# Kernel optimization log

Hardware: AMD Instinct MI355X
Metric: run time of the kernel (lower is better)

## Reference

```python
import jax, jax.numpy as jnp
import numpy as np

EPS = 1e-9
NEG_BIG = -1e9


def setup_inputs() -> dict:
    key = jax.random.key(0)
    kq, kk, kv, km = jax.random.split(key, 4)
    B, S, D = 2, 2048, 1024
    q = jax.random.normal(kq, (B, S, D), dtype=jnp.float32)
    k = jax.random.normal(kk, (B, S, D), dtype=jnp.float32)
    v = jax.random.normal(kv, (B, S, D), dtype=jnp.float32)
    mask = jax.random.randint(km, (S, S), 0, 2, dtype=jnp.int32)
    return {"q": q, "k": k, "v": v, "mask": mask, "num_heads": 16}


def _split_heads(x, num_heads):
    B, S, D = x.shape
    # [B, S, D] -> [B, H, S, dh]
    return x.reshape(B, S, num_heads, D // num_heads).transpose(0, 2, 1, 3)


def reference(q, k, v, mask, num_heads):
    B, S, D = q.shape
    dh = D // num_heads
    scale = dh ** (-0.5)
    qh = _split_heads(q, num_heads)  # [B,H,S,dh]
    kh = _split_heads(k, num_heads)
    vh = _split_heads(v, num_heads)
    # pairwise euclidean distance (cdist, p=2): sqrt(|q|^2 + |k|^2 - 2 q.k)
    q2 = jnp.sum(qh * qh, axis=-1)  # [B,H,S]
    k2 = jnp.sum(kh * kh, axis=-1)  # [B,H,S]
    qk = jnp.einsum("bhqd,bhkd->bhqk", qh, kh)
    d2 = q2[..., :, None] + k2[..., None, :] - 2.0 * qk
    dist = jnp.sqrt(jnp.maximum(d2, 0.0)) * scale  # [B,H,S,S]
    attn = 1.0 / (dist + EPS)
    attn = attn + mask.astype(jnp.float32)[None, None] * NEG_BIG
    attn = jax.nn.softmax(attn, axis=-1)
    # dropout is identity in eval / p=0.0
    x = jnp.einsum("bhqk,bhkd->bhqd", attn, vh)
    # [B,H,S,dh] -> [B,S,D]
    return x.transpose(0, 2, 1, 3).reshape(B, S, D)
```

## Files before the change

kernel.cpp:

```cpp
#include <hip/hip_runtime.h>
#include <hip/hip_bf16.h>
#include <math.h>

namespace {

constexpr int S  = 2048;
constexpr int D  = 1024;
constexpr int H  = 16;
constexpr int DH = 64;
constexpr int QB = 32;
constexpr int KT = 64;
constexpr float NEG_BIG = -1e9f;

typedef __attribute__((ext_vector_type(8))) short short8;
typedef __attribute__((ext_vector_type(4))) float f32x4;

union Frag {
  unsigned u[4];
  short8 v;
};

constexpr size_t ELEMS   = (size_t)2 * H * S * DH;
constexpr size_t OFF_KHI  = 0;
constexpr size_t OFF_KLO  = ELEMS * 2;
constexpr size_t OFF_VTHI = ELEMS * 4;
constexpr size_t OFF_VTLO = ELEMS * 6;
constexpr size_t OFF_K2   = ELEMS * 8;
constexpr size_t WS_NEED  = ELEMS * 8 + (size_t)2 * H * S * 4;

__device__ __forceinline__ unsigned fbits(float f) { return __float_as_uint(f); }
__device__ __forceinline__ unsigned packhi(unsigned a, unsigned b) {
  return (a >> 16) | (b & 0xFFFF0000u);
}
__device__ __forceinline__ void split2(float e, float o, unsigned& hi, unsigned& lo) {
  const unsigned ue = fbits(e), uo = fbits(o);
  hi = packhi(ue, uo);
  const float he = __uint_as_float(ue & 0xFFFF0000u);
  const float ho = __uint_as_float(uo & 0xFFFF0000u);
  lo = packhi(fbits(e - he), fbits(o - ho));
}

__device__ __forceinline__ unsigned bf16bits(float f) {
  __hip_bfloat16 h = __float2bfloat16(f);
  unsigned short us;
  __builtin_memcpy(&us, &h, 2);
  return (unsigned)us;
}
__device__ __forceinline__ unsigned pk2(float e, float o) {
  return bf16bits(e) | (bf16bits(o) << 16);
}

#define MFMA16 __builtin_amdgcn_mfma_f32_16x16x32_bf16


__global__ __launch_bounds__(256) void prep_k(const float* __restrict__ kin,
                                              short8* __restrict__ khi,
                                              short8* __restrict__ klo,
                                              float* __restrict__ k2) {
  const int t = blockIdx.x * 256 + (int)threadIdx.x;
  const int c = t & 7, h = (t >> 3) & 15, s = (t >> 7) & 2047, b = t >> 18;
  const float* p = kin + ((size_t)(b * S + s)) * D + h * DH + c * 8;
  float f[8];
  *(float4*)f       = *(const float4*)p;
  *(float4*)(f + 4) = *(const float4*)(p + 4);
  Frag hi, lo;
  float ss = 0.f;
#pragma unroll
  for (int w2 = 0; w2 < 4; ++w2) {
    split2(f[2 * w2], f[2 * w2 + 1], hi.u[w2], lo.u[w2]);
    ss += f[2 * w2] * f[2 * w2] + f[2 * w2 + 1] * f[2 * w2 + 1];
  }
  const size_t o8 = ((size_t)((b * 16 + h) * S + s)) * 8 + c;
  khi[o8] = hi.v;
  klo[o8] = lo.v;
  ss += __shfl_xor(ss, 1, 8);
  ss += __shfl_xor(ss, 2, 8);
  ss += __shfl_xor(ss, 4, 8);
  if (c == 0) k2[(b * 16 + h) * S + s] = ss;
}

__global__ __launch_bounds__(256) void prep_vt(const float* __restrict__ vin,
                                               short8* __restrict__ vthi,
                                               short8* __restrict__ vtlo) {
  __shared__ float Vs[64][65];
  const int blk = blockIdx.x;
  const int st = blk & 31, h = (blk >> 5) & 15, b = blk >> 9;
  const int t = (int)threadIdx.x;
  {
    const int r = t >> 2, cq = t & 3;
    const float* p = vin + ((size_t)(b * S + st * 64 + r)) * D + h * DH + cq * 16;
#pragma unroll
    for (int i = 0; i < 4; ++i)
      *(float4*)&Vs[r][cq * 16 + i * 4] = *(const float4*)(p + i * 4);
  }
  __syncthreads();
  const int d = t >> 2, sq = t & 3;
  Frag h0, h1, l0, l1;
#pragma unroll
  for (int j = 0; j < 4; ++j)
    split2(Vs[sq * 16 + 2 * j][d], Vs[sq * 16 + 2 * j + 1][d], h0.u[j], l0.u[j]);
#pragma unroll
  for (int j = 0; j < 4; ++j)
    split2(Vs[sq * 16 + 8 + 2 * j][d], Vs[sq * 16 + 8 + 2 * j + 1][d], h1.u[j], l1.u[j]);
  const size_t o8 = (((size_t)(b * 16 + h) * DH + d) * S + st * 64 + sq * 16) / 8;
  vthi[o8]     = h0.v;
  vthi[o8 + 1] = h1.v;
  vtlo[o8]     = l0.v;
  vtlo[o8 + 1] = l1.v;
}


__global__ __launch_bounds__(256, 2)
void euclid_attn_fast(const float* __restrict__ qg,
                      const int* __restrict__ maskg,
                      const short8* __restrict__ khi,
                      const short8* __restrict__ klo,
                      const short8* __restrict__ vthi,
                      const short8* __restrict__ vtlo,
                      const float* __restrict__ k2g,
                      float* __restrict__ outg) {
  const int bx = blockIdx.x;
  const int bh = blockIdx.y;
  const int b  = bh >> 4;
  const int tid  = (int)threadIdx.x;
  const int w    = tid >> 6;
  const int lane = tid & 63;
  const int x    = lane & 15;
  const int g    = lane >> 4;
  const int q0   = bx * QB;

  const float* Qb = qg + ((size_t)b * S + q0) * D + (bh & 15) * DH;

  const int idxk0 = (20 * g) * 4;
  const int idxe0 = (32 * (g & 1) + x) * 4;

  Frag Qhi[2][2], Qlo[2][2];
  float q2v[2];
#pragma unroll
  for (int nf = 0; nf < 2; ++nf) {
    float ss = 0.f;
#pragma unroll
    for (int s = 0; s < 2; ++s) {
      const float* p = Qb + (16 * nf + x) * D + 32 * s + 8 * g;
      float f[8];
      *(float4*)(f)     = *(const float4*)(p);
      *(float4*)(f + 4) = *(const float4*)(p + 4);
#pragma unroll
      for (int w2 = 0; w2 < 4; ++w2) {
        split2(f[2 * w2], f[2 * w2 + 1], Qhi[nf][s].u[w2], Qlo[nf][s].u[w2]);
        ss += f[2 * w2] * f[2 * w2] + f[2 * w2 + 1] * f[2 * w2 + 1];
      }
    }
    ss += __shfl_xor(ss, 16);
    ss += __shfl_xor(ss, 32);
    q2v[nf] = ss;
  }

  f32x4 acc[2][4] = {};
  float m_[2] = {-1e30f, -1e30f};
  float l_[2] = {0.f, 0.f};

  const int mrow0 = (q0 + x) * S;

  for (int t = 0; t < (S / KT) / 4; ++t) {
    const int k0 = (w + 4 * t) * KT;

    f32x4 dv[4][2];
    float rmax[2] = {-3e38f, -3e38f};

#pragma unroll
    for (int mf = 0; mf < 4; ++mf) {
      float mar[2][4];
#pragma unroll
      for (int nf = 0; nf < 2; ++nf) {
        const int4 mi =
            *(const int4*)(maskg + (size_t)mrow0 + 16 * nf * S + k0 + 16 * mf + 4 * g);
        mar[nf][0] = (float)mi.x; mar[nf][1] = (float)mi.y;
        mar[nf][2] = (float)mi.z; mar[nf][3] = (float)mi.w;
      }

      const size_t kb8 = ((size_t)bh * S + k0 + 16 * mf + x) * 8;
      Frag kh[2], kl[2];
      kh[0].v = khi[kb8 + g];
      kh[1].v = khi[kb8 + 4 + g];
      kl[0].v = klo[kb8 + g];
      kl[1].v = klo[kb8 + 4 + g];

      const float4 k2r = *(const float4*)(k2g + (size_t)bh * S + k0 + 16 * mf + 4 * g);
      const float k2a[4] = {k2r.x, k2r.y, k2r.z, k2r.w};

#pragma unroll
      for (int nf = 0; nf < 2; ++nf) {
        f32x4 d = {0.f, 0.f, 0.f, 0.f};
        d = MFMA16(kl[0].v, Qhi[nf][0].v, d, 0, 0, 0);
        d = MFMA16(kh[0].v, Qlo[nf][0].v, d, 0, 0, 0);
        d = MFMA16(kh[0].v, Qhi[nf][0].v, d, 0, 0, 0);
        d = MFMA16(kl[1].v, Qhi[nf][1].v, d, 0, 0, 0);
        d = MFMA16(kh[1].v, Qlo[nf][1].v, d, 0, 0, 0);
        d = MFMA16(kh[1].v, Qhi[nf][1].v, d, 0, 0, 0);
        dv[mf][nf] = d;
      }

#pragma unroll
      for (int nf = 0; nf < 2; ++nf)
#pragma unroll
        for (int r = 0; r < 4; ++r) {
          float d2 = q2v[nf] + k2a[r] - 2.f * dv[mf][nf][r];
          d2 = fmaxf(d2, 1e-8f);
          float a = 8.f * rsqrtf(d2);
          a = fmaf(mar[nf][r], NEG_BIG, a);
          dv[mf][nf][r] = a;
          rmax[nf] = fmaxf(rmax[nf], a);
        }
    }

    float corr_s[2];
#pragma unroll
    for (int nf = 0; nf < 2; ++nf) {
      float rm = rmax[nf];
      rm = fmaxf(rm, __shfl_xor(rm, 16));
      rm = fmaxf(rm, __shfl_xor(rm, 32));
      float mn   = fmaxf(m_[nf], rm);
      float corr = __expf(m_[nf] - mn);
      m_[nf] = mn;
      float rs = 0.f;
#pragma unroll
      for (int mf = 0; mf < 4; ++mf)
#pragma unroll
        for (int r = 0; r < 4; ++r) {
          float pp = __expf(dv[mf][nf][r] - mn);
          dv[mf][nf][r] = pp;
          rs += pp;
        }
      rs += __shfl_xor(rs, 16);
      rs += __shfl_xor(rs, 32);
      l_[nf] = l_[nf] * corr + rs;
      corr_s[nf] = corr;
    }

#pragma unroll
    for (int mo = 0; mo < 2; ++mo)
#pragma unroll
      for (int r = 0; r < 4; ++r) {
        float cT = __int_as_float(__builtin_amdgcn_ds_bpermute(
            idxk0 + 4 * r, __float_as_int(corr_s[mo])));
#pragma unroll
        for (int nv = 0; nv < 4; ++nv)
          acc[mo][nv][r] *= cT;
      }

    unsigned P2h[2][4][2], P2l[2][4][2];
#pragma unroll
    for (int nf = 0; nf < 2; ++nf)
#pragma unroll
      for (int mf = 0; mf < 4; ++mf)
#pragma unroll
        for (int c = 0; c < 2; ++c)
          split2(dv[mf][nf][2 * c], dv[mf][nf][2 * c + 1],
                 P2h[nf][mf][c], P2l[nf][mf][c]);

    Frag afh[2][2], afl[2][2];
    const bool upper = (g >= 2);
#pragma unroll
    for (int nf = 0; nf < 2; ++nf)
#pragma unroll
      for (int s2 = 0; s2 < 2; ++s2)
#pragma unroll
        for (int w4 = 0; w4 < 4; ++w4) {
          const int c = w4 & 1;
          const int idx = idxe0 + 64 * (w4 >> 1);
          int a0 = __builtin_amdgcn_ds_bpermute(idx, (int)P2h[nf][2 * s2][c]);
          int a1 = __builtin_amdgcn_ds_bpermute(idx, (int)P2h[nf][2 * s2 + 1][c]);
          afh[nf][s2].u[w4] = (unsigned)(upper ? a1 : a0);
          int b0 = __builtin_amdgcn_ds_bpermute(idx, (int)P2l[nf][2 * s2][c]);
          int b1 = __builtin_amdgcn_ds_bpermute(idx, (int)P2l[nf][2 * s2 + 1][c]);
          afl[nf][s2].u[w4] = (unsigned)(upper ? b1 : b0);
        }

#pragma unroll
    for (int nv = 0; nv < 4; ++nv)
#pragma unroll
      for (int s2 = 0; s2 < 2; ++s2) {
        const size_t vt8 =
            (((size_t)bh * DH + 16 * nv + x) * S + k0 + 32 * s2 + 8 * g) / 8;
        Frag vh, vl;
        vh.v = vthi[vt8];
        vl.v = vtlo[vt8];
#pragma unroll
        for (int mo = 0; mo < 2; ++mo) {
          f32x4 a = acc[mo][nv];
          a = MFMA16(afl[mo][s2].v, vh.v, a, 0, 0, 0);
          a = MFMA16(afh[mo][s2].v, vl.v, a, 0, 0, 0);
          a = MFMA16(afh[mo][s2].v, vh.v, a, 0, 0, 0);
          acc[mo][nv] = a;
        }
      }
  }

  __shared__ float accs[4][QB][DH];
  __shared__ float mls[4][2][QB];
#pragma unroll
  for (int mo = 0; mo < 2; ++mo)
#pragma unroll
    for (int nv = 0; nv < 4; ++nv)
#pragma unroll
      for (int r = 0; r < 4; ++r)
        accs[w][16 * mo + 4 * g + r][16 * nv + x] = acc[mo][nv][r];
  if (g == 0) {
#pragma unroll
    for (int nf = 0; nf < 2; ++nf) {
      mls[w][0][16 * nf + x] = m_[nf];
      mls[w][1][16 * nf + x] = l_[nf];
    }
  }
  __syncthreads();

  const int qq  = tid >> 3;
  const int dh0 = (tid & 7) * 8;
  float M = -3e38f;
#pragma unroll
  for (int ww = 0; ww < 4; ++ww) M = fmaxf(M, mls[ww][0][qq]);
  float L = 0.f;
  float sw[4];
#pragma unroll
  for (int ww = 0; ww < 4; ++ww) {
    sw[ww] = __expf(mls[ww][0][qq] - M);
    L += sw[ww] * mls[ww][1][qq];
  }
  const float inv = 1.f / L;
  float o[8] = {};
#pragma unroll
  for (int ww = 0; ww < 4; ++ww)
#pragma unroll
    for (int jj = 0; jj < 8; ++jj)
      o[jj] += sw[ww] * accs[ww][qq][dh0 + jj];
#pragma unroll
  for (int jj = 0; jj < 8; ++jj) o[jj] *= inv;
  float* op = outg + ((size_t)b * S + q0 + qq) * D + (bh & 15) * DH + dh0;
  *(float4*)(op)     = *(float4*)(o);
  *(float4*)(op + 4) = *(float4*)(o + 4);
}


__global__ __launch_bounds__(256, 2)
void euclid_attn_mfma(const float* __restrict__ qg,
                      const float* __restrict__ kg,
                      const float* __restrict__ vg,
                      const int*   __restrict__ maskg,
                      float*       __restrict__ outg) {
  const int bx = blockIdx.x;
  const int bh = blockIdx.y;
  const int b  = bh >> 4, h = bh & 15;
  const int tid  = (int)threadIdx.x;
  const int w    = tid >> 6;
  const int lane = tid & 63;
  const int x    = lane & 15;
  const int g    = lane >> 4;
  const int q0   = bx * QB;

  const float* Qb = qg + ((size_t)b * S + q0) * D + h * DH;
  const float* Kb = kg + (size_t)b * S * D + h * DH;
  const float* Vb = vg + (size_t)b * S * D + h * DH;

  const int idxk0 = (20 * g) * 4;
  const int idxe0 = (32 * (g & 1) + x) * 4;

  Frag Qhi[2][2], Qlo[2][2];
  float q2v[2];
#pragma unroll
  for (int nf = 0; nf < 2; ++nf) {
    float ss = 0.f;
#pragma unroll
    for (int s = 0; s < 2; ++s) {
      const float* p = Qb + (16 * nf + x) * D + 32 * s + 8 * g;
      float f[8];
      *(float4*)(f)     = *(const float4*)(p);
      *(float4*)(f + 4) = *(const float4*)(p + 4);
#pragma unroll
      for (int w2 = 0; w2 < 4; ++w2) {
        float e = f[2*w2], o = f[2*w2+1];
        unsigned hw = pk2(e, o);
        Qhi[nf][s].u[w2] = hw;
        float he = __uint_as_float(hw << 16);
        float ho = __uint_as_float(hw & 0xFFFF0000u);
        Qlo[nf][s].u[w2] = pk2(e - he, o - ho);
        ss += e * e + o * o;
      }
    }
    ss += __shfl_xor(ss, 16);
    ss += __shfl_xor(ss, 32);
    q2v[nf] = ss;
  }

  f32x4 acc[2][4] = {};
  float m_[2] = {-1e30f, -1e30f};
  float l_[2] = {0.f, 0.f};

  const int mrow0 = (q0 + x) * S;

  for (int t = 0; t < (S / KT) / 4; ++t) {
    const int k0 = (w + 4 * t) * KT;

    f32x4 dv[4][2];
    float rmax[2] = {-3e38f, -3e38f};

#pragma unroll
    for (int mf = 0; mf < 4; ++mf) {
      float msk[2][4];
#pragma unroll
      for (int nf = 0; nf < 2; ++nf)
#pragma unroll
        for (int r = 0; r < 4; ++r)
          msk[nf][r] =
              (float)maskg[mrow0 + 16 * nf * S + k0 + 16 * mf + 4 * g + r];

      const float* kp = Kb + (k0 + 16 * mf + x) * D + 8 * g;
      float f[16];
      *(float4*)(f)      = *(const float4*)(kp);
      *(float4*)(f + 4)  = *(const float4*)(kp + 4);
      *(float4*)(f + 8)  = *(const float4*)(kp + 32);
      *(float4*)(f + 12) = *(const float4*)(kp + 36);
      Frag khi[2], klo[2];
      float ss = 0.f;
#pragma unroll
      for (int s = 0; s < 2; ++s)
#pragma unroll
        for (int w2 = 0; w2 < 4; ++w2) {
          float e = f[8*s + 2*w2], o = f[8*s + 2*w2 + 1];
          unsigned hw = pk2(e, o);
          khi[s].u[w2] = hw;
          float he = __uint_as_float(hw << 16);
          float ho = __uint_as_float(hw & 0xFFFF0000u);
          klo[s].u[w2] = pk2(e - he, o - ho);
          ss += e * e + o * o;
        }
      ss += __shfl_xor(ss, 16);
      ss += __shfl_xor(ss, 32);
      float k2r[4];
#pragma unroll
      for (int r = 0; r < 4; ++r)
        k2r[r] = __int_as_float(
            __builtin_amdgcn_ds_bpermute(idxk0 + 4 * r, __float_as_int(ss)));

#pragma unroll
      for (int nf = 0; nf < 2; ++nf) {
        f32x4 d = {0.f, 0.f, 0.f, 0.f};
        d = MFMA16(klo[0].v, Qhi[nf][0].v, d, 0, 0, 0);
        d = MFMA16(khi[0].v, Qlo[nf][0].v, d, 0, 0, 0);
        d = MFMA16(khi[0].v, Qhi[nf][0].v, d, 0, 0, 0);
        d = MFMA16(klo[1].v, Qhi[nf][1].v, d, 0, 0, 0);
        d = MFMA16(khi[1].v, Qlo[nf][1].v, d, 0, 0, 0);
        d = MFMA16(khi[1].v, Qhi[nf][1].v, d, 0, 0, 0);
        dv[mf][nf] = d;
      }

#pragma unroll
      for (int nf = 0; nf < 2; ++nf)
#pragma unroll
        for (int r = 0; r < 4; ++r) {
          float d2 = q2v[nf] + k2r[r] - 2.f * dv[mf][nf][r];
          d2 = fmaxf(d2, 1e-8f);
          float a = 8.f * rsqrtf(d2);
          a = fmaf(msk[nf][r], NEG_BIG, a);
          dv[mf][nf][r] = a;
          rmax[nf] = fmaxf(rmax[nf], a);
        }
    }

    float corr_s[2];
#pragma unroll
    for (int nf = 0; nf < 2; ++nf) {
      float rm = rmax[nf];
      rm = fmaxf(rm, __shfl_xor(rm, 16));
      rm = fmaxf(rm, __shfl_xor(rm, 32));
      float mn   = fmaxf(m_[nf], rm);
      float corr = __expf(m_[nf] - mn);
      m_[nf] = mn;
      float rs = 0.f;
#pragma unroll
      for (int mf = 0; mf < 4; ++mf)
#pragma unroll
        for (int r = 0; r < 4; ++r) {
          float pp = __expf(dv[mf][nf][r] - mn);
          dv[mf][nf][r] = pp;
          rs += pp;
        }
      rs += __shfl_xor(rs, 16);
      rs += __shfl_xor(rs, 32);
      l_[nf] = l_[nf] * corr + rs;
      corr_s[nf] = corr;
    }

#pragma unroll
    for (int mo = 0; mo < 2; ++mo)
#pragma unroll
      for (int r = 0; r < 4; ++r) {
        float cT = __int_as_float(__builtin_amdgcn_ds_bpermute(
            idxk0 + 4 * r, __float_as_int(corr_s[mo])));
#pragma unroll
        for (int nv = 0; nv < 4; ++nv)
          acc[mo][nv][r] *= cT;
      }

    unsigned P2h[2][4][2], P2l[2][4][2];
#pragma unroll
    for (int nf = 0; nf < 2; ++nf)
#pragma unroll
      for (int mf = 0; mf < 4; ++mf)
#pragma unroll
        for (int c = 0; c < 2; ++c) {
          float p0 = dv[mf][nf][2*c], p1 = dv[mf][nf][2*c+1];
          unsigned hw = pk2(p0, p1);
          P2h[nf][mf][c] = hw;
          float he = __uint_as_float(hw << 16);
          float ho = __uint_as_float(hw & 0xFFFF0000u);
          P2l[nf][mf][c] = pk2(p0 - he, p1 - ho);
        }

    Frag afh[2][2], afl[2][2];
    const bool upper = (g >= 2);
#pragma unroll
    for (int nf = 0; nf < 2; ++nf)
#pragma unroll
      for (int s2 = 0; s2 < 2; ++s2)
#pragma unroll
        for (int w4 = 0; w4 < 4; ++w4) {
          const int c = w4 & 1;
          const int idx = idxe0 + 64 * (w4 >> 1);
          int a0 = __builtin_amdgcn_ds_bpermute(idx, (int)P2h[nf][2*s2][c]);
          int a1 = __builtin_amdgcn_ds_bpermute(idx, (int)P2h[nf][2*s2+1][c]);
          afh[nf][s2].u[w4] = (unsigned)(upper ? a1 : a0);
          int b0 = __builtin_amdgcn_ds_bpermute(idx, (int)P2l[nf][2*s2][c]);
          int b1 = __builtin_amdgcn_ds_bpermute(idx, (int)P2l[nf][2*s2+1][c]);
          afl[nf][s2].u[w4] = (unsigned)(upper ? b1 : b0);
        }

#pragma unroll
    for (int nv = 0; nv < 4; ++nv)
#pragma unroll
      for (int s2 = 0; s2 < 2; ++s2) {
        const float* vp = Vb + (k0 + 32 * s2 + 8 * g) * D + 16 * nv + x;
        float f[8];
#pragma unroll
        for (int j = 0; j < 8; ++j) f[j] = vp[j * D];
        Frag vh, vl;
#pragma unroll
        for (int w2 = 0; w2 < 4; ++w2) {
          float e = f[2*w2], o = f[2*w2+1];
          unsigned hw = pk2(e, o);
          vh.u[w2] = hw;
          float he = __uint_as_float(hw << 16);
          float ho = __uint_as_float(hw & 0xFFFF0000u);
          vl.u[w2] = pk2(e - he, o - ho);
        }
#pragma unroll
        for (int mo = 0; mo < 2; ++mo) {
          f32x4 a = acc[mo][nv];
          a = MFMA16(afl[mo][s2].v, vh.v, a, 0, 0, 0);
          a = MFMA16(afh[mo][s2].v, vl.v, a, 0, 0, 0);
          a = MFMA16(afh[mo][s2].v, vh.v, a, 0, 0, 0);
          acc[mo][nv] = a;
        }
      }
  }

  __shared__ float accs[4][QB][DH];
  __shared__ float mls[4][2][QB];
#pragma unroll
  for (int mo = 0; mo < 2; ++mo)
#pragma unroll
    for (int nv = 0; nv < 4; ++nv)
#pragma unroll
      for (int r = 0; r < 4; ++r)
        accs[w][16 * mo + 4 * g + r][16 * nv + x] = acc[mo][nv][r];
  if (g == 0) {
#pragma unroll
    for (int nf = 0; nf < 2; ++nf) {
      mls[w][0][16 * nf + x] = m_[nf];
      mls[w][1][16 * nf + x] = l_[nf];
    }
  }
  __syncthreads();

  const int qq  = tid >> 3;
  const int dh0 = (tid & 7) * 8;
  float M = -3e38f;
#pragma unroll
  for (int ww = 0; ww < 4; ++ww) M = fmaxf(M, mls[ww][0][qq]);
  float L = 0.f;
  float sw[4];
#pragma unroll
  for (int ww = 0; ww < 4; ++ww) {
    sw[ww] = __expf(mls[ww][0][qq] - M);
    L += sw[ww] * mls[ww][1][qq];
  }
  const float inv = 1.f / L;
  float o[8] = {};
#pragma unroll
  for (int ww = 0; ww < 4; ++ww)
#pragma unroll
    for (int jj = 0; jj < 8; ++jj)
      o[jj] += sw[ww] * accs[ww][qq][dh0 + jj];
#pragma unroll
  for (int jj = 0; jj < 8; ++jj) o[jj] *= inv;
  float* op = outg + ((size_t)b * S + q0 + qq) * D + h * DH + dh0;
  *(float4*)(op)     = *(float4*)(o);
  *(float4*)(op + 4) = *(float4*)(o + 4);
}

}

extern "C" void kernel_launch(void* const* d_in, const int* in_sizes, int n_in,
                              void* d_out, int out_size, void* d_ws, size_t ws_size,
                              hipStream_t stream) {
  const float* q    = (const float*)d_in[0];
  const float* k    = (const float*)d_in[1];
  const float* v    = (const float*)d_in[2];
  const int*   mask = (const int*)d_in[3];
  float* out = (float*)d_out;

  const int B = in_sizes[0] / (S * D);
  dim3 grid(S / QB, B * H);
  dim3 block(256);

  if (B == 2 && d_ws != nullptr && ws_size >= WS_NEED) {
    char* ws = (char*)d_ws;
    short8* khi  = (short8*)(ws + OFF_KHI);
    short8* klo  = (short8*)(ws + OFF_KLO);
    short8* vthi = (short8*)(ws + OFF_VTHI);
    short8* vtlo = (short8*)(ws + OFF_VTLO);
    float*  k2   = (float*)(ws + OFF_K2);
    prep_k<<<2048, 256, 0, stream>>>(k, khi, klo, k2);
    prep_vt<<<1024, 256, 0, stream>>>(v, vthi, vtlo);
    euclid_attn_fast<<<grid, block, 0, stream>>>(q, mask, khi, klo, vthi, vtlo,
                                                 k2, out);
  } else {
    euclid_attn_mfma<<<grid, block, 0, stream>>>(q, k, v, mask, out);
  }
}
```

Baseline: 413.5 us.

## Give each wave its own 16 query rows over full key range, drop cross-wave merge

The fast attention kernel now assigns each of the four waves a separate 16-row query tile and has it sweep all keys, instead of four waves splitting the key range for a shared 32-row tile. This removes the shared-memory partial-softmax merge and its barrier, halves per-wave register state, and raises the launch-bounds occupancy hint from 2 to 4 blocks. It also adds a lazy rescale that skips the running-max correction when no new max exceeds the old one by more than 8. In exchange, each K/V fragment load now feeds only one query tile, so K/V reuse per load drops and global/L2 traffic for K and V rises.

```diff
diff --git a/kernel.cpp b/kernel.cpp
--- a/kernel.cpp
+++ b/kernel.cpp
@@ -8,7 +8,6 @@
 constexpr int D  = 1024;
 constexpr int H  = 16;
 constexpr int DH = 64;
-constexpr int QB = 32;
 constexpr int KT = 64;
 constexpr float NEG_BIG = -1e9f;
 
@@ -110,15 +109,15 @@
 }
 
 
-__global__ __launch_bounds__(256, 2)
-void euclid_attn_fast(const float* __restrict__ qg,
-                      const int* __restrict__ maskg,
-                      const short8* __restrict__ khi,
-                      const short8* __restrict__ klo,
-                      const short8* __restrict__ vthi,
-                      const short8* __restrict__ vtlo,
-                      const float* __restrict__ k2g,
-                      float* __restrict__ outg) {
+__global__ __launch_bounds__(256, 4)
+void euclid_attn_v2(const float* __restrict__ qg,
+                    const int* __restrict__ maskg,
+                    const short8* __restrict__ khi,
+                    const short8* __restrict__ klo,
+                    const short8* __restrict__ vthi,
+                    const short8* __restrict__ vtlo,
+                    const float* __restrict__ k2g,
+                    float* __restrict__ outg) {
   const int bx = blockIdx.x;
   const int bh = blockIdx.y;
   const int b  = bh >> 4;
@@ -127,57 +126,50 @@
   const int lane = tid & 63;
   const int x    = lane & 15;
   const int g    = lane >> 4;
-  const int q0   = bx * QB;
+  const int q0   = bx * 64 + w * 16;
 
   const float* Qb = qg + ((size_t)b * S + q0) * D + (bh & 15) * DH;
 
   const int idxk0 = (20 * g) * 4;
   const int idxe0 = (32 * (g & 1) + x) * 4;
 
-  Frag Qhi[2][2], Qlo[2][2];
-  float q2v[2];
-#pragma unroll
-  for (int nf = 0; nf < 2; ++nf) {
+  Frag Qhi[2], Qlo[2];
+  float q2v;
+  {
     float ss = 0.f;
 #pragma unroll
     for (int s = 0; s < 2; ++s) {
-      const float* p = Qb + (16 * nf + x) * D + 32 * s + 8 * g;
+      const float* p = Qb + x * D + 32 * s + 8 * g;
       float f[8];
       *(float4*)(f)     = *(const float4*)(p);
       *(float4*)(f + 4) = *(const float4*)(p + 4);
 #pragma unroll
       for (int w2 = 0; w2 < 4; ++w2) {
-        split2(f[2 * w2], f[2 * w2 + 1], Qhi[nf][s].u[w2], Qlo[nf][s].u[w2]);
+        split2(f[2 * w2], f[2 * w2 + 1], Qhi[s].u[w2], Qlo[s].u[w2]);
         ss += f[2 * w2] * f[2 * w2] + f[2 * w2 + 1] * f[2 * w2 + 1];
       }
     }
     ss += __shfl_xor(ss, 16);
     ss += __shfl_xor(ss, 32);
-    q2v[nf] = ss;
-  }
-
-  f32x4 acc[2][4] = {};
-  float m_[2] = {-1e30f, -1e30f};
-  float l_[2] = {0.f, 0.f};
-
-  const int mrow0 = (q0 + x) * S;
-
-  for (int t = 0; t < (S / KT) / 4; ++t) {
-    const int k0 = (w + 4 * t) * KT;
-
-    f32x4 dv[4][2];
-    float rmax[2] = {-3e38f, -3e38f};
+    q2v = ss;
+  }
+
+  f32x4 acc[4] = {};
+  float m_ = -1e30f;
+  float l_ = 0.f;
+
+  const size_t mrow0 = (size_t)(q0 + x) * S;
+
+  for (int t = 0; t < S / KT; ++t) {
+    const int k0 = t * KT;
+
+    f32x4 dv[4];
+    float rmax = -3e38f;
 
 #pragma unroll
     for (int mf = 0; mf < 4; ++mf) {
-      float mar[2][4];
-#pragma unroll
-      for (int nf = 0; nf < 2; ++nf) {
-        const int4 mi =
-            *(const int4*)(maskg + (size_t)mrow0 + 16 * nf * S + k0 + 16 * mf + 4 * g);
-        mar[nf][0] = (float)mi.x; mar[nf][1] = (float)mi.y;
-        mar[nf][2] = (float)mi.z; mar[nf][3] = (float)mi.w;
-      }
+      const int4 mi = *(const int4*)(maskg + mrow0 + k0 + 16 * mf + 4 * g);
+      float mar[4] = {(float)mi.x, (float)mi.y, (float)mi.z, (float)mi.w};
 
       const size_t kb8 = ((size_t)bh * S + k0 + 16 * mf + x) * 8;
       Frag kh[2], kl[2];
@@ -189,93 +181,82 @@
       const float4 k2r = *(const float4*)(k2g + (size_t)bh * S + k0 + 16 * mf + 4 * g);
       const float k2a[4] = {k2r.x, k2r.y, k2r.z, k2r.w};
 
-#pragma unroll
-      for (int nf = 0; nf < 2; ++nf) {
-        f32x4 d = {0.f, 0.f, 0.f, 0.f};
-        d = MFMA16(kl[0].v, Qhi[nf][0].v, d, 0, 0, 0);
-        d = MFMA16(kh[0].v, Qlo[nf][0].v, d, 0, 0, 0);
-        d = MFMA16(kh[0].v, Qhi[nf][0].v, d, 0, 0, 0);
-        d = MFMA16(kl[1].v, Qhi[nf][1].v, d, 0, 0, 0);
-        d = MFMA16(kh[1].v, Qlo[nf][1].v, d, 0, 0, 0);
-        d = MFMA16(kh[1].v, Qhi[nf][1].v, d, 0, 0, 0);
-        dv[mf][nf] = d;
-      }
-
-#pragma unroll
-      for (int nf = 0; nf < 2; ++nf)
-#pragma unroll
-        for (int r = 0; r < 4; ++r) {
-          float d2 = q2v[nf] + k2a[r] - 2.f * dv[mf][nf][r];
-          d2 = fmaxf(d2, 1e-8f);
-          float a = 8.f * rsqrtf(d2);
-          a = fmaf(mar[nf][r], NEG_BIG, a);
-          dv[mf][nf][r] = a;
-          rmax[nf] = fmaxf(rmax[nf], a);
-        }
-    }
-
-    float corr_s[2];
-#pragma unroll
-    for (int nf = 0; nf < 2; ++nf) {
-      float rm = rmax[nf];
-      rm = fmaxf(rm, __shfl_xor(rm, 16));
-      rm = fmaxf(rm, __shfl_xor(rm, 32));
-      float mn   = fmaxf(m_[nf], rm);
-      float corr = __expf(m_[nf] - mn);
-      m_[nf] = mn;
-      float rs = 0.f;
-#pragma unroll
-      for (int mf = 0; mf < 4; ++mf)
-#pragma unroll
-        for (int r = 0; r < 4; ++r) {
-          float pp = __expf(dv[mf][nf][r] - mn);
-          dv[mf][nf][r] = pp;
-          rs += pp;
-        }
-      rs += __shfl_xor(rs, 16);
-      rs += __shfl_xor(rs, 32);
-      l_[nf] = l_[nf] * corr + rs;
-      corr_s[nf] = corr;
-    }
-
-#pragma unroll
-    for (int mo = 0; mo < 2; ++mo)
+      f32x4 d = {0.f, 0.f, 0.f, 0.f};
+      d = MFMA16(kl[0].v, Qhi[0].v, d, 0, 0, 0);
+      d = MFMA16(kh[0].v, Qlo[0].v, d, 0, 0, 0);
+      d = MFMA16(kh[0].v, Qhi[0].v, d, 0, 0, 0);
+      d = MFMA16(kl[1].v, Qhi[1].v, d, 0, 0, 0);
+      d = MFMA16(kh[1].v, Qlo[1].v, d, 0, 0, 0);
+      d = MFMA16(kh[1].v, Qhi[1].v, d, 0, 0, 0);
+
+#pragma unroll
+      for (int r = 0; r < 4; ++r) {
+        float d2 = q2v + k2a[r] - 2.f * d[r];
+        d2 = fmaxf(d2, 1e-8f);
+        float a = 8.f * rsqrtf(d2);
+        a = fmaf(mar[r], NEG_BIG, a);
+        d[r] = a;
+        rmax = fmaxf(rmax, a);
+      }
+      dv[mf] = d;
+    }
+
+    float rm = rmax;
+    rm = fmaxf(rm, __shfl_xor(rm, 16));
+    rm = fmaxf(rm, __shfl_xor(rm, 32));
+    float corr = 1.f;
+    const bool need = !__all(rm <= m_ + 8.f);
+    if (need) {
+      const float mn = fmaxf(m_, rm);
+      corr = __expf(m_ - mn);
+      m_ = mn;
+    }
+    float rs = 0.f;
+#pragma unroll
+    for (int mf = 0; mf < 4; ++mf)
+#pragma unroll
+      for (int r = 0; r < 4; ++r) {
+        float pp = __expf(dv[mf][r] - m_);
+        dv[mf][r] = pp;
+        rs += pp;
+      }
+    rs += __shfl_xor(rs, 16);
+    rs += __shfl_xor(rs, 32);
+    l_ = l_ * corr + rs;
+
+    if (need) {
 #pragma unroll
       for (int r = 0; r < 4; ++r) {
         float cT = __int_as_float(__builtin_amdgcn_ds_bpermute(
-            idxk0 + 4 * r, __float_as_int(corr_s[mo])));
+            idxk0 + 4 * r, __float_as_int(corr)));
 #pragma unroll
         for (int nv = 0; nv < 4; ++nv)
-          acc[mo][nv][r] *= cT;
-      }
-
-    unsigned P2h[2][4][2], P2l[2][4][2];
-#pragma unroll
-    for (int nf = 0; nf < 2; ++nf)
-#pragma unroll
-      for (int mf = 0; mf < 4; ++mf)
-#pragma unroll
-        for (int c = 0; c < 2; ++c)
-          split2(dv[mf][nf][2 * c], dv[mf][nf][2 * c + 1],
-                 P2h[nf][mf][c], P2l[nf][mf][c]);
-
-    Frag afh[2][2], afl[2][2];
+          acc[nv][r] *= cT;
+      }
+    }
+
+    unsigned P2h[4][2], P2l[4][2];
+#pragma unroll
+    for (int mf = 0; mf < 4; ++mf)
+#pragma unroll
+      for (int c = 0; c < 2; ++c)
+        split2(dv[mf][2 * c], dv[mf][2 * c + 1], P2h[mf][c], P2l[mf][c]);
+
+    Frag afh[2], afl[2];
     const bool upper = (g >= 2);
 #pragma unroll
-    for (int nf = 0; nf < 2; ++nf)
-#pragma unroll
-      for (int s2 = 0; s2 < 2; ++s2)
-#pragma unroll
-        for (int w4 = 0; w4 < 4; ++w4) {
-          const int c = w4 & 1;
-          const int idx = idxe0 + 64 * (w4 >> 1);
-          int a0 = __builtin_amdgcn_ds_bpermute(idx, (int)P2h[nf][2 * s2][c]);
-          int a1 = __builtin_amdgcn_ds_bpermute(idx, (int)P2h[nf][2 * s2 + 1][c]);
-          afh[nf][s2].u[w4] = (unsigned)(upper ? a1 : a0);
-          int b0 = __builtin_amdgcn_ds_bpermute(idx, (int)P2l[nf][2 * s2][c]);
-          int b1 = __builtin_amdgcn_ds_bpermute(idx, (int)P2l[nf][2 * s2 + 1][c]);
-          afl[nf][s2].u[w4] = (unsigned)(upper ? b1 : b0);
-        }
+    for (int s2 = 0; s2 < 2; ++s2)
+#pragma unroll
+      for (int w4 = 0; w4 < 4; ++w4) {
+        const int c = w4 & 1;
+        const int idx = idxe0 + 64 * (w4 >> 1);
+        int a0 = __builtin_amdgcn_ds_bpermute(idx, (int)P2h[2 * s2][c]);
+        int a1 = __builtin_amdgcn_ds_bpermute(idx, (int)P2h[2 * s2 + 1][c]);
+        afh[s2].u[w4] = (unsigned)(upper ? a1 : a0);
+        int b0 = __builtin_amdgcn_ds_bpermute(idx, (int)P2l[2 * s2][c]);
+        int b1 = __builtin_amdgcn_ds_bpermute(idx, (int)P2l[2 * s2 + 1][c]);
+        afl[s2].u[w4] = (unsigned)(upper ? b1 : b0);
+      }
 
 #pragma unroll
     for (int nv = 0; nv < 4; ++nv)
@@ -286,59 +267,24 @@
         Frag vh, vl;
         vh.v = vthi[vt8];
         vl.v = vtlo[vt8];
-#pragma unroll
-        for (int mo = 0; mo < 2; ++mo) {
-          f32x4 a = acc[mo][nv];
-          a = MFMA16(afl[mo][s2].v, vh.v, a, 0, 0, 0);
-          a = MFMA16(afh[mo][s2].v, vl.v, a, 0, 0, 0);
-          a = MFMA16(afh[mo][s2].v, vh.v, a, 0, 0, 0);
-          acc[mo][nv] = a;
-        }
-      }
-  }
-
-  __shared__ float accs[4][QB][DH];
-  __shared__ float mls[4][2][QB];
-#pragma unroll
-  for (int mo = 0; mo < 2; ++mo)
+        f32x4 a = acc[nv];
+        a = MFMA16(afl[s2].v, vh.v, a, 0, 0, 0);
+        a = MFMA16(afh[s2].v, vl.v, a, 0, 0, 0);
+        a = MFMA16(afh[s2].v, vh.v, a, 0, 0, 0);
+        acc[nv] = a;
+      }
+  }
+
+#pragma unroll
+  for (int r = 0; r < 4; ++r) {
+    const float lT = __int_as_float(
+        __builtin_amdgcn_ds_bpermute(idxk0 + 4 * r, __float_as_int(l_)));
+    const float inv = 1.f / lT;
+    float* op = outg + ((size_t)b * S + q0 + 4 * g + r) * D + (bh & 15) * DH + x;
 #pragma unroll
     for (int nv = 0; nv < 4; ++nv)
-#pragma unroll
-      for (int r = 0; r < 4; ++r)
-        accs[w][16 * mo + 4 * g + r][16 * nv + x] = acc[mo][nv][r];
-  if (g == 0) {
-#pragma unroll
-    for (int nf = 0; nf < 2; ++nf) {
-      mls[w][0][16 * nf + x] = m_[nf];
-      mls[w][1][16 * nf + x] = l_[nf];
-    }
-  }
-  __syncthreads();
-
-  const int qq  = tid >> 3;
-  const int dh0 = (tid & 7) * 8;
-  float M = -3e38f;
-#pragma unroll
-  for (int ww = 0; ww < 4; ++ww) M = fmaxf(M, mls[ww][0][qq]);
-  float L = 0.f;
-  float sw[4];
-#pragma unroll
-  for (int ww = 0; ww < 4; ++ww) {
-    sw[ww] = __expf(mls[ww][0][qq] - M);
-    L += sw[ww] * mls[ww][1][qq];
-  }
-  const float inv = 1.f / L;
-  float o[8] = {};
-#pragma unroll
-  for (int ww = 0; ww < 4; ++ww)
-#pragma unroll
-    for (int jj = 0; jj < 8; ++jj)
-      o[jj] += sw[ww] * accs[ww][qq][dh0 + jj];
-#pragma unroll
-  for (int jj = 0; jj < 8; ++jj) o[jj] *= inv;
-  float* op = outg + ((size_t)b * S + q0 + qq) * D + (bh & 15) * DH + dh0;
-  *(float4*)(op)     = *(float4*)(o);
-  *(float4*)(op + 4) = *(float4*)(o + 4);
+      op[16 * nv] = acc[nv][r] * inv;
+  }
 }
 
 
@@ -356,7 +302,7 @@
   const int lane = tid & 63;
   const int x    = lane & 15;
   const int g    = lane >> 4;
-  const int q0   = bx * QB;
+  const int q0   = bx * 32;
 
   const float* Qb = qg + ((size_t)b * S + q0) * D + h * DH;
   const float* Kb = kg + (size_t)b * S * D + h * DH;
@@ -564,8 +510,8 @@
       }
   }
 
-  __shared__ float accs[4][QB][DH];
-  __shared__ float mls[4][2][QB];
+  __shared__ float accs[4][32][DH];
+  __shared__ float mls[4][2][32];
 #pragma unroll
   for (int mo = 0; mo < 2; ++mo)
 #pragma unroll
@@ -620,8 +566,6 @@
   float* out = (float*)d_out;
 
   const int B = in_sizes[0] / (S * D);
-  dim3 grid(S / QB, B * H);
-  dim3 block(256);
 
   if (B == 2 && d_ws != nullptr && ws_size >= WS_NEED) {
     char* ws = (char*)d_ws;
@@ -632,9 +576,11 @@
     float*  k2   = (float*)(ws + OFF_K2);
     prep_k<<<2048, 256, 0, stream>>>(k, khi, klo, k2);
     prep_vt<<<1024, 256, 0, stream>>>(v, vthi, vtlo);
-    euclid_attn_fast<<<grid, block, 0, stream>>>(q, mask, khi, klo, vthi, vtlo,
-                                                 k2, out);
+    dim3 grid(S / 64, B * H);
+    euclid_attn_v2<<<grid, dim3(256), 0, stream>>>(q, mask, khi, klo, vthi,
+                                                   vtlo, k2, out);
   } else {
-    euclid_attn_mfma<<<grid, block, 0, stream>>>(q, k, v, mask, out);
-  }
-}
+    dim3 grid(S / 32, B * H);
+    euclid_attn_mfma<<<grid, dim3(256), 0, stream>>>(q, k, v, mask, out);
+  }
+}
```

New measurement: 628.8 us. 1.52x slower.

## Raise occupancy, halve epilogue LDS, and skip lazy softmax rescales

Applied to the files above, without the earlier changes.

Raises the launch bound of the fast kernel from 2 to 4 blocks per CU. The cross-wave reduction buffer is halved to [4][32][32] and the epilogue now runs in two passes over the head dimension, so the kernel needs less LDS. The online softmax now rescales the accumulator only when the new row max exceeds the stored max by more than 8 (a lazy rescale) and skips the bpermute-and-multiply step otherwise. The intent is more waves in flight and less per-tile work. The risks are register spills under the tighter bound and extra syncs in the epilogue.

```diff
diff --git a/kernel.cpp b/kernel.cpp
--- a/kernel.cpp
+++ b/kernel.cpp
@@ -8,7 +8,6 @@
 constexpr int D  = 1024;
 constexpr int H  = 16;
 constexpr int DH = 64;
-constexpr int QB = 32;
 constexpr int KT = 64;
 constexpr float NEG_BIG = -1e9f;
 
@@ -110,7 +109,7 @@
 }
 
 
-__global__ __launch_bounds__(256, 2)
+__global__ __launch_bounds__(256, 4)
 void euclid_attn_fast(const float* __restrict__ qg,
                       const int* __restrict__ maskg,
                       const short8* __restrict__ khi,
@@ -127,7 +126,7 @@
   const int lane = tid & 63;
   const int x    = lane & 15;
   const int g    = lane >> 4;
-  const int q0   = bx * QB;
+  const int q0   = bx * 32;
 
   const float* Qb = qg + ((size_t)b * S + q0) * D + (bh & 15) * DH;
 
@@ -160,7 +159,7 @@
   float m_[2] = {-1e30f, -1e30f};
   float l_[2] = {0.f, 0.f};
 
-  const int mrow0 = (q0 + x) * S;
+  const size_t mrow0 = (size_t)(q0 + x) * S;
 
   for (int t = 0; t < (S / KT) / 4; ++t) {
     const int k0 = (w + 4 * t) * KT;
@@ -174,7 +173,7 @@
 #pragma unroll
       for (int nf = 0; nf < 2; ++nf) {
         const int4 mi =
-            *(const int4*)(maskg + (size_t)mrow0 + 16 * nf * S + k0 + 16 * mf + 4 * g);
+            *(const int4*)(maskg + mrow0 + 16 * nf * S + k0 + 16 * mf + 4 * g);
         mar[nf][0] = (float)mi.x; mar[nf][1] = (float)mi.y;
         mar[nf][2] = (float)mi.z; mar[nf][3] = (float)mi.w;
       }
@@ -215,39 +214,46 @@
     }
 
     float corr_s[2];
+    bool needr = false;
 #pragma unroll
     for (int nf = 0; nf < 2; ++nf) {
       float rm = rmax[nf];
       rm = fmaxf(rm, __shfl_xor(rm, 16));
       rm = fmaxf(rm, __shfl_xor(rm, 32));
-      float mn   = fmaxf(m_[nf], rm);
-      float corr = __expf(m_[nf] - mn);
-      m_[nf] = mn;
+      float corr = 1.f;
+      if (!__all(rm <= m_[nf] + 8.f)) {
+        const float mn = fmaxf(m_[nf], rm);
+        corr = __expf(m_[nf] - mn);
+        m_[nf] = mn;
+        needr = true;
+      }
+      corr_s[nf] = corr;
       float rs = 0.f;
 #pragma unroll
       for (int mf = 0; mf < 4; ++mf)
 #pragma unroll
         for (int r = 0; r < 4; ++r) {
-          float pp = __expf(dv[mf][nf][r] - mn);
+          float pp = __expf(dv[mf][nf][r] - m_[nf]);
           dv[mf][nf][r] = pp;
           rs += pp;
         }
       rs += __shfl_xor(rs, 16);
       rs += __shfl_xor(rs, 32);
       l_[nf] = l_[nf] * corr + rs;
-      corr_s[nf] = corr;
-    }
-
-#pragma unroll
-    for (int mo = 0; mo < 2; ++mo)
-#pragma unroll
-      for (int r = 0; r < 4; ++r) {
-        float cT = __int_as_float(__builtin_amdgcn_ds_bpermute(
-            idxk0 + 4 * r, __float_as_int(corr_s[mo])));
-#pragma unroll
-        for (int nv = 0; nv < 4; ++nv)
-          acc[mo][nv][r] *= cT;
-      }
+    }
+
+    if (needr) {
+#pragma unroll
+      for (int mo = 0; mo < 2; ++mo)
+#pragma unroll
+        for (int r = 0; r < 4; ++r) {
+          float cT = __int_as_float(__builtin_amdgcn_ds_bpermute(
+              idxk0 + 4 * r, __float_as_int(corr_s[mo])));
+#pragma unroll
+          for (int nv = 0; nv < 4; ++nv)
+            acc[mo][nv][r] *= cT;
+        }
+    }
 
     unsigned P2h[2][4][2], P2l[2][4][2];
 #pragma unroll
@@ -297,12 +303,13 @@
       }
   }
 
-  __shared__ float accs[4][QB][DH];
-  __shared__ float mls[4][2][QB];
+  __shared__ float accs[4][32][32];
+  __shared__ float mls[4][2][32];
+
 #pragma unroll
   for (int mo = 0; mo < 2; ++mo)
 #pragma unroll
-    for (int nv = 0; nv < 4; ++nv)
+    for (int nv = 0; nv < 2; ++nv)
 #pragma unroll
       for (int r = 0; r < 4; ++r)
         accs[w][16 * mo + 4 * g + r][16 * nv + x] = acc[mo][nv][r];
@@ -315,8 +322,8 @@
   }
   __syncthreads();
 
-  const int qq  = tid >> 3;
-  const int dh0 = (tid & 7) * 8;
+  const int qq = tid >> 3;
+  const int d4 = (tid & 7) * 4;
   float M = -3e38f;
 #pragma unroll
   for (int ww = 0; ww < 4; ++ww) M = fmaxf(M, mls[ww][0][qq]);
@@ -328,17 +335,41 @@
     L += sw[ww] * mls[ww][1][qq];
   }
   const float inv = 1.f / L;
-  float o[8] = {};
-#pragma unroll
-  for (int ww = 0; ww < 4; ++ww)
-#pragma unroll
-    for (int jj = 0; jj < 8; ++jj)
-      o[jj] += sw[ww] * accs[ww][qq][dh0 + jj];
-#pragma unroll
-  for (int jj = 0; jj < 8; ++jj) o[jj] *= inv;
-  float* op = outg + ((size_t)b * S + q0 + qq) * D + (bh & 15) * DH + dh0;
-  *(float4*)(op)     = *(float4*)(o);
-  *(float4*)(op + 4) = *(float4*)(o + 4);
+
+  float* orow = outg + ((size_t)b * S + q0 + qq) * D + (bh & 15) * DH;
+  {
+    float o[4] = {};
+#pragma unroll
+    for (int ww = 0; ww < 4; ++ww)
+#pragma unroll
+      for (int jj = 0; jj < 4; ++jj)
+        o[jj] += sw[ww] * accs[ww][qq][d4 + jj];
+#pragma unroll
+    for (int jj = 0; jj < 4; ++jj) o[jj] *= inv;
+    *(float4*)(orow + d4) = *(float4*)(o);
+  }
+  __syncthreads();
+
+#pragma unroll
+  for (int mo = 0; mo < 2; ++mo)
+#pragma unroll
+    for (int nv = 2; nv < 4; ++nv)
+#pragma unroll
+      for (int r = 0; r < 4; ++r)
+        accs[w][16 * mo + 4 * g + r][16 * (nv - 2) + x] = acc[mo][nv][r];
+  __syncthreads();
+
+  {
+    float o[4] = {};
+#pragma unroll
+    for (int ww = 0; ww < 4; ++ww)
+#pragma unroll
+      for (int jj = 0; jj < 4; ++jj)
+        o[jj] += sw[ww] * accs[ww][qq][d4 + jj];
+#pragma unroll
+    for (int jj = 0; jj < 4; ++jj) o[jj] *= inv;
+    *(float4*)(orow + 32 + d4) = *(float4*)(o);
+  }
 }
 
 
@@ -356,7 +387,7 @@
   const int lane = tid & 63;
   const int x    = lane & 15;
   const int g    = lane >> 4;
-  const int q0   = bx * QB;
+  const int q0   = bx * 32;
 
   const float* Qb = qg + ((size_t)b * S + q0) * D + h * DH;
   const float* Kb = kg + (size_t)b * S * D + h * DH;
@@ -564,8 +595,8 @@
       }
   }
 
-  __shared__ float accs[4][QB][DH];
-  __shared__ float mls[4][2][QB];
+  __shared__ float accs[4][32][DH];
+  __shared__ float mls[4][2][32];
 #pragma unroll
   for (int mo = 0; mo < 2; ++mo)
 #pragma unroll
@@ -620,7 +651,7 @@
   float* out = (float*)d_out;
 
   const int B = in_sizes[0] / (S * D);
-  dim3 grid(S / QB, B * H);
+  dim3 grid(S / 32, B * H);
   dim3 block(256);
 
   if (B == 2 && d_ws != nullptr && ws_size >= WS_NEED) {
```

Measured after the change: 573.1 us. +38.6%, slower.
